# Performance work log

Hardware: AMD Instinct MI355X
Metric: run time of the kernel (lower is better)

The kernel has to match this reference:

```python
import jax, jax.numpy as jnp
import numpy as np

N = 50000          # nodes
E = 800000         # edges (before self-loops)
IN_CH = 128
HID = 64
HEADS = 4
NEG_SLOPE = 0.2    # PyG GATConv default negative_slope


def _gat_conv(x, W, a_src, a_dst, bias, src, dst, heads, out_ch):
    """PyG-style GATConv (concat=True). src/dst already include self-loops."""
    n = x.shape[0]
    h = (x @ W).reshape(n, heads, out_ch)                 # [N,H,C]
    # per-node attention halves: a_src . h_i  and  a_dst . h_i
    es = (h * a_src[None]).sum(-1)                        # [N,H]
    ed = (h * a_dst[None]).sum(-1)                        # [N,H]
    logits = jax.nn.leaky_relu(es[src] + ed[dst], NEG_SLOPE)   # [Etot,H]
    # segment softmax over incoming edges of each dst node
    m = jax.ops.segment_max(logits, dst, num_segments=n)       # [N,H]
    m = jnp.where(jnp.isfinite(m), m, jnp.zeros_like(m))
    p = jnp.exp(logits - m[dst])                               # [Etot,H]
    s = jax.ops.segment_sum(p, dst, num_segments=n)            # [N,H]
    att = p / (s[dst] + 1e-16)                                 # [Etot,H]
    msg = h[src] * att[..., None]                              # [Etot,H,C]
    out = jax.ops.segment_sum(msg, dst, num_segments=n)        # [N,H,C]
    return out.reshape(n, heads * out_ch) + bias


def setup_inputs() -> dict:
    key = jax.random.key(0)
    ks = jax.random.split(key, 12)
    x = jax.random.normal(ks[0], (N, IN_CH), dtype=jnp.float32)
    edge_index = jax.random.randint(ks[1], (2, E), 0, N, dtype=jnp.int32)
    def glorot(k, shape, fan_in):
        return jax.random.normal(k, shape, dtype=jnp.float32) * (1.0 / np.sqrt(fan_in))
    return {
        "x": x,
        "W1": glorot(ks[2], (IN_CH, HEADS * HID), IN_CH),
        "a_src1": glorot(ks[3], (HEADS, HID), HID),
        "a_dst1": glorot(ks[4], (HEADS, HID), HID),
        "b1": jnp.zeros((HEADS * HID,), dtype=jnp.float32),
        "W2": glorot(ks[5], (HEADS * HID, HID), HEADS * HID),
        "a_src2": glorot(ks[6], (1, HID), HID),
        "a_dst2": glorot(ks[7], (1, HID), HID),
        "b2": jnp.zeros((HID,), dtype=jnp.float32),
        "Wo": glorot(ks[8], (HID, 1), HID),
        "bo": jnp.zeros((1,), dtype=jnp.float32),
        "edge_index": edge_index,
    }


def reference(x, W1, a_src1, a_dst1, b1, W2, a_src2, a_dst2, b2, Wo, bo, edge_index):
    n = x.shape[0]
    loops = jnp.arange(n, dtype=edge_index.dtype)          # add_self_loops=True (PyG default)
    src = jnp.concatenate([edge_index[0], loops])
    dst = jnp.concatenate([edge_index[1], loops])
    h = jax.nn.elu(_gat_conv(x, W1, a_src1, a_dst1, b1, src, dst, HEADS, HID))
    # dropout inactive in eval mode
    h = jax.nn.elu(_gat_conv(h, W2, a_src2, a_dst2, b2, src, dst, 1, HID))
    return (h @ Wo + bo).squeeze(-1)                       # [N]
```

## Files before the change

### kernel.cpp

```cpp
#include <hip/hip_runtime.h>
#include <cmath>

#define LRELU_SLOPE 0.2f

static inline int cdiv_h(int a, int b){ return (a + b - 1) / b; }

__device__ __forceinline__ float dev_lrelu(float x){ return x > 0.f ? x : LRELU_SLOPE * x; }
__device__ __forceinline__ float dev_elu(float x){ return x > 0.f ? x : expm1f(x); }

__device__ __forceinline__ unsigned short f2bf(float f){
  unsigned int u = __float_as_uint(f);
  u = (u + 0x7FFFu + ((u >> 16) & 1u)) >> 16;
  return (unsigned short)u;
}
__device__ __forceinline__ float bf2f_lo(unsigned int u){
  return __uint_as_float(u << 16);
}
__device__ __forceinline__ float bf2f_hi(unsigned int u){
  return __uint_as_float(u & 0xFFFF0000u);
}

__device__ __forceinline__ float edge_w(float logit){
  return __expf(fminf(logit, 80.f));
}

typedef __attribute__((ext_vector_type(8))) short bf16x8;
typedef __attribute__((ext_vector_type(4))) float f32x4;

#define CNT_STRIDE 16

__global__ void prep_kernel(const float* __restrict__ W1, unsigned short* __restrict__ W1T,
                            const float* __restrict__ W2, unsigned short* __restrict__ W2T,
                            int* __restrict__ cnt, int n)
{
  int b = blockIdx.x, t = threadIdx.x;
  if (b < 128){
    int i = b * 256 + t;
    int k = i >> 8, c = i & 255;
    W1T[(size_t)c * 128 + k] = f2bf(W1[i]);
  } else if (b < 192){
    int i = (b - 128) * 256 + t;
    int k = i >> 6, c = i & 63;
    W2T[(size_t)c * 256 + k] = f2bf(W2[i]);
  } else {
    int i = (b - 192) * 256 + t;
    if (i < n) cnt[(size_t)i * CNT_STRIDE] = 1;
  }
}


__global__ void scan_blocks_kernel(const int* __restrict__ cnt, int* __restrict__ rowptr,
                                   int n, int* __restrict__ bsum){
  __shared__ int sd[256];
  int idx = blockIdx.x * 256 + threadIdx.x;
  int v = (idx < n) ? cnt[(size_t)idx * CNT_STRIDE] : 0;
  sd[threadIdx.x] = v;
  __syncthreads();
  #pragma unroll
  for (int off = 1; off < 256; off <<= 1){
    int x = (threadIdx.x >= off) ? sd[threadIdx.x - off] : 0;
    __syncthreads();
    sd[threadIdx.x] += x;
    __syncthreads();
  }
  if (idx < n) rowptr[idx] = sd[threadIdx.x] - v;
  if (threadIdx.x == 255) bsum[blockIdx.x] = sd[255];
}

__global__ void scan_add_kernel(int* __restrict__ rowptr, int n, const int* __restrict__ bsum,
                                int total, unsigned short* __restrict__ col){
  __shared__ int red[256];
  int t = threadIdx.x;
  int p = 0;
  for (int k = t; k < (int)blockIdx.x; k += 256) p += bsum[k];
  red[t] = p;
  __syncthreads();
  #pragma unroll
  for (int off = 128; off > 0; off >>= 1){
    if (t < off) red[t] += red[t + off];
    __syncthreads();
  }
  int prefix = red[0];
  int idx = blockIdx.x * 256 + t;
  if (idx < n){
    int v = rowptr[idx] + prefix;
    rowptr[idx] = v;
    col[v] = (unsigned short)idx;
  }
  if (idx == 0) rowptr[n] = total;
}

__global__ void scatter_kernel(const int* __restrict__ ei, const int* __restrict__ rank,
                               const int* __restrict__ rowptr, int e, unsigned short* __restrict__ col){
  int i = blockIdx.x * blockDim.x + threadIdx.x;
  if (i >= e) return;
  int s = ei[i], d = ei[e + i];
  col[rowptr[d] + rank[i]] = (unsigned short)s;
}

__launch_bounds__(256)
__global__ void gemm1_mfma_kernel(const float* __restrict__ A, const unsigned short* __restrict__ BT,
                                  unsigned short* __restrict__ Cb,
                                  const float* __restrict__ a_src, const float* __restrict__ a_dst,
                                  float* __restrict__ es, float* __restrict__ ed,
                                  int M, int K, int GB,
                                  const int* __restrict__ hist_dst, int He,
                                  int* __restrict__ cnt, int* __restrict__ rank)
{
  constexpr int BN = 256, NSUB = 16, H = 4;
  constexpr int LDK = 40;
  __shared__ short As[64 * LDK];
  __shared__ short Bs[BN * LDK];
  const int tid = threadIdx.x;

  if (blockIdx.x >= GB){
    int i = (blockIdx.x - GB) * 256 + tid;
    if (i < He){
      int d = hist_dst[i];
      rank[i] = atomicAdd(&cnt[(size_t)d * CNT_STRIDE], 1);
    }
    return;
  }

  const int bm = blockIdx.x;
  const int wave = tid >> 6, lane = tid & 63;
  const int lm = lane & 15, quad = lane >> 4;
  const int arow = tid >> 2, kc8 = (tid & 3) * 8;
  const int gm_a = bm * 64 + arow;

  f32x4 acc[NSUB];
  #pragma unroll
  for (int i = 0; i < NSUB; i++) acc[i] = (f32x4){0.f, 0.f, 0.f, 0.f};

  for (int k0 = 0; k0 < K; k0 += 32){
    unsigned short a8[8];
    float4 t0 = {0,0,0,0}, t1 = {0,0,0,0};
    if (gm_a < M){
      t0 = *(const float4*)&A[(size_t)gm_a * K + k0 + kc8];
      t1 = *(const float4*)&A[(size_t)gm_a * K + k0 + kc8 + 4];
    }
    a8[0] = f2bf(t0.x); a8[1] = f2bf(t0.y); a8[2] = f2bf(t0.z); a8[3] = f2bf(t0.w);
    a8[4] = f2bf(t1.x); a8[5] = f2bf(t1.y); a8[6] = f2bf(t1.z); a8[7] = f2bf(t1.w);
    uint4 b8[4];
    #pragma unroll
    for (int rep = 0; rep < 4; rep++){
      int brow = rep * 64 + arow;
      b8[rep] = *(const uint4*)&BT[(size_t)brow * K + k0 + kc8];
    }
    __syncthreads();
    *(uint4*)&As[arow * LDK + kc8] = *(uint4*)a8;
    #pragma unroll
    for (int rep = 0; rep < 4; rep++)
      *(uint4*)&Bs[(rep * 64 + arow) * LDK + kc8] = b8[rep];
    __syncthreads();
    bf16x8 af = *(const bf16x8*)&As[(wave * 16 + lm) * LDK + quad * 8];
    #pragma unroll
    for (int nb = 0; nb < NSUB; nb++){
      bf16x8 bfr = *(const bf16x8*)&Bs[(nb * 16 + lm) * LDK + quad * 8];
      acc[nb] = __builtin_amdgcn_mfma_f32_16x16x32_bf16(af, bfr, acc[nb], 0, 0, 0);
    }
  }

  float asv[NSUB], adv[NSUB];
  #pragma unroll
  for (int nb = 0; nb < NSUB; nb++){
    asv[nb] = a_src[nb * 16 + lm];
    adv[nb] = a_dst[nb * 16 + lm];
  }
  #pragma unroll
  for (int r = 0; r < 4; r++){
    int gm = bm * 64 + wave * 16 + quad * 4 + r;
    if (gm < M){
      #pragma unroll
      for (int nb = 0; nb < NSUB; nb++)
        Cb[(size_t)gm * BN + nb * 16 + lm] = f2bf(acc[nb][r]);
    }
    #pragma unroll
    for (int h = 0; h < H; h++){
      float ps = 0.f, pd = 0.f;
      #pragma unroll
      for (int nbh = 0; nbh < 4; nbh++){
        int nb = h * 4 + nbh;
        float a = acc[nb][r];
        ps += a * asv[nb];
        pd += a * adv[nb];
      }
      #pragma unroll
      for (int off = 1; off < 16; off <<= 1){
        ps += __shfl_xor(ps, off, 64);
        pd += __shfl_xor(pd, off, 64);
      }
      if (lm == 0 && gm < M){
        es[(size_t)gm * H + h] = ps;
        ed[(size_t)gm * H + h] = pd;
      }
    }
  }
}

__launch_bounds__(256)
__global__ void gemm2_mfma_kernel(const unsigned short* __restrict__ A, const unsigned short* __restrict__ BT,
                                  unsigned short* __restrict__ Cb,
                                  const float* __restrict__ a_src, const float* __restrict__ a_dst,
                                  float* __restrict__ es, float* __restrict__ ed,
                                  int M, int K)
{
  constexpr int BN = 64, NSUB = 4;
  constexpr int LDK = 40;
  __shared__ short As[128 * LDK];
  __shared__ short Bs[64 * LDK];
  const int tid = threadIdx.x;
  const int bm = blockIdx.x;
  const int wave = tid >> 6, lane = tid & 63;
  const int lm = lane & 15, quad = lane >> 4;
  const int arow = tid >> 2, kc8 = (tid & 3) * 8;
  const int gm_a0 = bm * 128 + arow;
  const int gm_a1 = gm_a0 + 64;

  f32x4 acc0[NSUB], acc1[NSUB];
  #pragma unroll
  for (int i = 0; i < NSUB; i++){
    acc0[i] = (f32x4){0.f, 0.f, 0.f, 0.f};
    acc1[i] = (f32x4){0.f, 0.f, 0.f, 0.f};
  }

  for (int k0 = 0; k0 < K; k0 += 32){
    uint4 a0 = make_uint4(0,0,0,0), a1 = make_uint4(0,0,0,0);
    if (gm_a0 < M) a0 = *(const uint4*)&A[(size_t)gm_a0 * K + k0 + kc8];
    if (gm_a1 < M) a1 = *(const uint4*)&A[(size_t)gm_a1 * K + k0 + kc8];
    uint4 b = *(const uint4*)&BT[(size_t)arow * K + k0 + kc8];
    __syncthreads();
    *(uint4*)&As[arow * LDK + kc8] = a0;
    *(uint4*)&As[(64 + arow) * LDK + kc8] = a1;
    *(uint4*)&Bs[arow * LDK + kc8] = b;
    __syncthreads();
    bf16x8 af0 = *(const bf16x8*)&As[(wave * 16 + lm) * LDK + quad * 8];
    bf16x8 af1 = *(const bf16x8*)&As[(64 + wave * 16 + lm) * LDK + quad * 8];
    #pragma unroll
    for (int nb = 0; nb < NSUB; nb++){
      bf16x8 bfr = *(const bf16x8*)&Bs[(nb * 16 + lm) * LDK + quad * 8];
      acc0[nb] = __builtin_amdgcn_mfma_f32_16x16x32_bf16(af0, bfr, acc0[nb], 0, 0, 0);
      acc1[nb] = __builtin_amdgcn_mfma_f32_16x16x32_bf16(af1, bfr, acc1[nb], 0, 0, 0);
    }
  }

  float asv[NSUB], adv[NSUB];
  #pragma unroll
  for (int nb = 0; nb < NSUB; nb++){
    asv[nb] = a_src[nb * 16 + lm];
    adv[nb] = a_dst[nb * 16 + lm];
  }
  #pragma unroll
  for (int half = 0; half < 2; half++){
    #pragma unroll
    for (int r = 0; r < 4; r++){
      int gm = bm * 128 + half * 64 + wave * 16 + quad * 4 + r;
      float ps = 0.f, pd = 0.f;
      #pragma unroll
      for (int nb = 0; nb < NSUB; nb++){
        float a = half ? acc1[nb][r] : acc0[nb][r];
        if (gm < M) Cb[(size_t)gm * BN + nb * 16 + lm] = f2bf(a);
        ps += a * asv[nb];
        pd += a * adv[nb];
      }
      #pragma unroll
      for (int off = 1; off < 16; off <<= 1){
        ps += __shfl_xor(ps, off, 64);
        pd += __shfl_xor(pd, off, 64);
      }
      if (lm == 0 && gm < M){
        es[gm] = ps;
        ed[gm] = pd;
      }
    }
  }
}

__global__ void agg1_kernel(const unsigned short* __restrict__ h1b, const float* __restrict__ es,
                            const float* __restrict__ ed,
                            const int* __restrict__ rowptr, const unsigned short* __restrict__ col,
                            const float* __restrict__ b1, unsigned short* __restrict__ out1b, int n)
{
  int node = blockIdx.x * 8 + (threadIdx.x >> 5);
  if (node >= n) return;
  int r = threadIdx.x & 31;
  int h = r >> 3;
  float edh = ed[node * 4 + h];
  int start = rowptr[node], end = rowptr[node + 1];
  float l = 0.f;
  float a0=0.f,a1=0.f,a2=0.f,a3=0.f,a4=0.f,a5=0.f,a6=0.f,a7=0.f;
  int j = start;
  for (; j + 3 < end; j += 4){
    int s0 = col[j], s1 = col[j+1], s2 = col[j+2], s3 = col[j+3];
    float e0 = es[s0*4 + h], e1 = es[s1*4 + h], e2 = es[s2*4 + h], e3 = es[s3*4 + h];
    uint4 r0 = *(const uint4*)&h1b[(size_t)s0 * 256 + r * 8];
    uint4 r1 = *(const uint4*)&h1b[(size_t)s1 * 256 + r * 8];
    uint4 r2 = *(const uint4*)&h1b[(size_t)s2 * 256 + r * 8];
    uint4 r3 = *(const uint4*)&h1b[(size_t)s3 * 256 + r * 8];
    float w0 = edge_w(dev_lrelu(e0 + edh));
    float w1 = edge_w(dev_lrelu(e1 + edh));
    float w2 = edge_w(dev_lrelu(e2 + edh));
    float w3 = edge_w(dev_lrelu(e3 + edh));
    l += w0 + w1 + w2 + w3;
    a0 += bf2f_lo(r0.x)*w0 + bf2f_lo(r1.x)*w1 + bf2f_lo(r2.x)*w2 + bf2f_lo(r3.x)*w3;
    a1 += bf2f_hi(r0.x)*w0 + bf2f_hi(r1.x)*w1 + bf2f_hi(r2.x)*w2 + bf2f_hi(r3.x)*w3;
    a2 += bf2f_lo(r0.y)*w0 + bf2f_lo(r1.y)*w1 + bf2f_lo(r2.y)*w2 + bf2f_lo(r3.y)*w3;
    a3 += bf2f_hi(r0.y)*w0 + bf2f_hi(r1.y)*w1 + bf2f_hi(r2.y)*w2 + bf2f_hi(r3.y)*w3;
    a4 += bf2f_lo(r0.z)*w0 + bf2f_lo(r1.z)*w1 + bf2f_lo(r2.z)*w2 + bf2f_lo(r3.z)*w3;
    a5 += bf2f_hi(r0.z)*w0 + bf2f_hi(r1.z)*w1 + bf2f_hi(r2.z)*w2 + bf2f_hi(r3.z)*w3;
    a6 += bf2f_lo(r0.w)*w0 + bf2f_lo(r1.w)*w1 + bf2f_lo(r2.w)*w2 + bf2f_lo(r3.w)*w3;
    a7 += bf2f_hi(r0.w)*w0 + bf2f_hi(r1.w)*w1 + bf2f_hi(r2.w)*w2 + bf2f_hi(r3.w)*w3;
  }
  for (; j < end; j++){
    int s0 = col[j];
    float w0 = edge_w(dev_lrelu(es[s0*4 + h] + edh));
    uint4 r0 = *(const uint4*)&h1b[(size_t)s0 * 256 + r * 8];
    l += w0;
    a0 += bf2f_lo(r0.x)*w0; a1 += bf2f_hi(r0.x)*w0;
    a2 += bf2f_lo(r0.y)*w0; a3 += bf2f_hi(r0.y)*w0;
    a4 += bf2f_lo(r0.z)*w0; a5 += bf2f_hi(r0.z)*w0;
    a6 += bf2f_lo(r0.w)*w0; a7 += bf2f_hi(r0.w)*w0;
  }
  float inv = 1.f / l;
  float4 bA = *(const float4*)&b1[r * 8];
  float4 bB = *(const float4*)&b1[r * 8 + 4];
  uint4 o;
  o.x = (unsigned int)f2bf(dev_elu(a0*inv + bA.x)) | ((unsigned int)f2bf(dev_elu(a1*inv + bA.y)) << 16);
  o.y = (unsigned int)f2bf(dev_elu(a2*inv + bA.z)) | ((unsigned int)f2bf(dev_elu(a3*inv + bA.w)) << 16);
  o.z = (unsigned int)f2bf(dev_elu(a4*inv + bB.x)) | ((unsigned int)f2bf(dev_elu(a5*inv + bB.y)) << 16);
  o.w = (unsigned int)f2bf(dev_elu(a6*inv + bB.z)) | ((unsigned int)f2bf(dev_elu(a7*inv + bB.w)) << 16);
  *(uint4*)&out1b[(size_t)node * 256 + r * 8] = o;
}

__global__ void agg2_kernel(const unsigned short* __restrict__ h2b, const float* __restrict__ es,
                            const float* __restrict__ ed,
                            const int* __restrict__ rowptr, const unsigned short* __restrict__ col,
                            const float* __restrict__ b2, const float* __restrict__ Wo,
                            const float* __restrict__ bo, float* __restrict__ out, int n)
{
  int node = blockIdx.x * 16 + (threadIdx.x >> 4);
  if (node >= n) return;
  int r = threadIdx.x & 15;
  float edh = ed[node];
  int start = rowptr[node], end = rowptr[node + 1];
  float l = 0.f;
  float a0=0.f,a1=0.f,a2=0.f,a3=0.f;
  int j = start;
  for (; j + 3 < end; j += 4){
    int s0 = col[j], s1 = col[j+1], s2 = col[j+2], s3 = col[j+3];
    float e0 = es[s0], e1 = es[s1], e2 = es[s2], e3 = es[s3];
    uint2 r0 = *(const uint2*)&h2b[(size_t)s0 * 64 + r * 4];
    uint2 r1 = *(const uint2*)&h2b[(size_t)s1 * 64 + r * 4];
    uint2 r2 = *(const uint2*)&h2b[(size_t)s2 * 64 + r * 4];
    uint2 r3 = *(const uint2*)&h2b[(size_t)s3 * 64 + r * 4];
    float w0 = edge_w(dev_lrelu(e0 + edh));
    float w1 = edge_w(dev_lrelu(e1 + edh));
    float w2 = edge_w(dev_lrelu(e2 + edh));
    float w3 = edge_w(dev_lrelu(e3 + edh));
    l += w0 + w1 + w2 + w3;
    a0 += bf2f_lo(r0.x)*w0 + bf2f_lo(r1.x)*w1 + bf2f_lo(r2.x)*w2 + bf2f_lo(r3.x)*w3;
    a1 += bf2f_hi(r0.x)*w0 + bf2f_hi(r1.x)*w1 + bf2f_hi(r2.x)*w2 + bf2f_hi(r3.x)*w3;
    a2 += bf2f_lo(r0.y)*w0 + bf2f_lo(r1.y)*w1 + bf2f_lo(r2.y)*w2 + bf2f_lo(r3.y)*w3;
    a3 += bf2f_hi(r0.y)*w0 + bf2f_hi(r1.y)*w1 + bf2f_hi(r2.y)*w2 + bf2f_hi(r3.y)*w3;
  }
  for (; j < end; j++){
    int s0 = col[j];
    float w0 = edge_w(dev_lrelu(es[s0] + edh));
    uint2 r0 = *(const uint2*)&h2b[(size_t)s0 * 64 + r * 4];
    l += w0;
    a0 += bf2f_lo(r0.x)*w0; a1 += bf2f_hi(r0.x)*w0;
    a2 += bf2f_lo(r0.y)*w0; a3 += bf2f_hi(r0.y)*w0;
  }
  float inv = 1.f / l;
  float4 bb = *(const float4*)&b2[r * 4];
  float4 wo = *(const float4*)&Wo[r * 4];
  float t = dev_elu(a0*inv + bb.x) * wo.x
          + dev_elu(a1*inv + bb.y) * wo.y
          + dev_elu(a2*inv + bb.z) * wo.z
          + dev_elu(a3*inv + bb.w) * wo.w;
  #pragma unroll
  for (int off = 1; off < 16; off <<= 1) t += __shfl_xor(t, off, 64);
  if (r == 0) out[node] = t + bo[0];
}

extern "C" void kernel_launch(void* const* d_in, const int* in_sizes, int n_in,
                              void* d_out, int out_size, void* d_ws, size_t ws_size,
                              hipStream_t stream)
{
  const float* x    = (const float*)d_in[0];
  const float* W1   = (const float*)d_in[1];
  const float* a_s1 = (const float*)d_in[2];
  const float* a_d1 = (const float*)d_in[3];
  const float* b1   = (const float*)d_in[4];
  const float* W2   = (const float*)d_in[5];
  const float* a_s2 = (const float*)d_in[6];
  const float* a_d2 = (const float*)d_in[7];
  const float* b2   = (const float*)d_in[8];
  const float* Wo   = (const float*)d_in[9];
  const float* bo   = (const float*)d_in[10];
  const int*   ei   = (const int*)d_in[11];

  const int Nn = in_sizes[0] / 128;
  const int E  = in_sizes[11] / 2;
  const int ET = E + Nn;

  size_t off = 0;
  auto carve = [&](size_t bytes) -> void* {
    void* p = (char*)d_ws + off;
    off += (bytes + 255) & ~(size_t)255;
    return p;
  };
  unsigned short* h1b   = (unsigned short*)carve((size_t)Nn * 256 * sizeof(unsigned short));
  unsigned short* out1b = (unsigned short*)carve((size_t)Nn * 256 * sizeof(unsigned short));
  unsigned short* h2b   = (unsigned short*)carve((size_t)Nn * 64 * sizeof(unsigned short));
  unsigned short* W1T   = (unsigned short*)carve((size_t)128 * 256 * sizeof(unsigned short));
  unsigned short* W2T   = (unsigned short*)carve((size_t)256 * 64 * sizeof(unsigned short));
  float* es1    = (float*)carve((size_t)Nn * 4 * sizeof(float));
  float* ed1    = (float*)carve((size_t)Nn * 4 * sizeof(float));
  float* es2    = (float*)carve((size_t)Nn * sizeof(float));
  float* ed2    = (float*)carve((size_t)Nn * sizeof(float));
  int*   cnt    = (int*)carve((size_t)Nn * CNT_STRIDE * sizeof(int));
  int*   rowptr = (int*)carve((size_t)(Nn + 1) * sizeof(int));
  int*   rank   = (int*)carve((size_t)E * sizeof(int));
  int*   bsum   = (int*)carve(256 * sizeof(int));
  unsigned short* col = (unsigned short*)carve((size_t)ET * sizeof(unsigned short));
  float* out = (float*)d_out;

  int deg_blocks = cdiv_h(Nn, 256);
  prep_kernel<<<192 + deg_blocks, 256, 0, stream>>>(W1, W1T, W2, W2T, cnt, Nn);

  int GB1 = cdiv_h(Nn, 64);
  int HB  = cdiv_h(E, 256);
  gemm1_mfma_kernel<<<GB1 + HB, 256, 0, stream>>>(
      x, W1T, h1b, a_s1, a_d1, es1, ed1, Nn, 128, GB1, ei + E, E, cnt, rank);

  int nb = cdiv_h(Nn, 256);
  scan_blocks_kernel<<<nb, 256, 0, stream>>>(cnt, rowptr, Nn, bsum);
  scan_add_kernel<<<nb, 256, 0, stream>>>(rowptr, Nn, bsum, ET, col);
  scatter_kernel<<<cdiv_h(E, 256), 256, 0, stream>>>(ei, rank, rowptr, E, col);

  agg1_kernel<<<cdiv_h(Nn, 8), 256, 0, stream>>>(h1b, es1, ed1, rowptr, col, b1, out1b, Nn);

  gemm2_mfma_kernel<<<cdiv_h(Nn, 128), 256, 0, stream>>>(
      out1b, W2T, h2b, a_s2, a_d2, es2, ed2, Nn, 256);
  agg2_kernel<<<cdiv_h(Nn, 16), 256, 0, stream>>>(h2b, es2, ed2, rowptr, col, b2, Wo, bo, out, Nn);
}
```

Measured before the change: 255.8 us.

## Build CSR with chunked shared-memory histograms instead of global atomics

Replaces the global-atomic degree counting and per-edge rank with a chunked approach. Per-chunk shared-memory histograms over node quarters are written as 16-bit counts, then a per-node scan across chunks gives offsets, and a placement pass recomputes local ranks with shared atomics. The histogram no longer overlaps with gemm1 and needs two edge passes plus an NC×N count array. Both edge passes run a 4×NC grid, so every edge is read four times. Self-loop placement uses the +1 offset.

Result: slower. 280.8 us (+9.8%).

```diff
diff --git a/kernel.cpp b/kernel.cpp
--- a/kernel.cpp
+++ b/kernel.cpp
@@ -27,33 +27,102 @@
 typedef __attribute__((ext_vector_type(8))) short bf16x8;
 typedef __attribute__((ext_vector_type(4))) float f32x4;
 
-#define CNT_STRIDE 16
+#define CE 8192
+#define QS 12500
 
 __global__ void prep_kernel(const float* __restrict__ W1, unsigned short* __restrict__ W1T,
-                            const float* __restrict__ W2, unsigned short* __restrict__ W2T,
-                            int* __restrict__ cnt, int n)
+                            const float* __restrict__ W2, unsigned short* __restrict__ W2T)
 {
   int b = blockIdx.x, t = threadIdx.x;
   if (b < 128){
     int i = b * 256 + t;
     int k = i >> 8, c = i & 255;
     W1T[(size_t)c * 128 + k] = f2bf(W1[i]);
-  } else if (b < 192){
+  } else {
     int i = (b - 128) * 256 + t;
     int k = i >> 6, c = i & 63;
     W2T[(size_t)c * 256 + k] = f2bf(W2[i]);
-  } else {
-    int i = (b - 192) * 256 + t;
-    if (i < n) cnt[(size_t)i * CNT_STRIDE] = 1;
-  }
-}
-
-
-__global__ void scan_blocks_kernel(const int* __restrict__ cnt, int* __restrict__ rowptr,
+  }
+}
+
+
+__global__ void csr_count_kernel(const int* __restrict__ dst, int e, int n,
+                                 unsigned short* __restrict__ cnt)
+{
+  __shared__ unsigned int lc[QS];
+  int c = blockIdx.x, q = blockIdx.y;
+  int lo = q * QS;
+  int hi = min(lo + QS, n);
+  int width = hi - lo;
+  for (int k = threadIdx.x; k < width; k += 256) lc[k] = 0;
+  __syncthreads();
+  int i0 = c * CE, i1 = min(i0 + CE, e);
+  for (int i = i0 + threadIdx.x; i < i1; i += 256){
+    int d = dst[i];
+    if (d >= lo && d < hi) atomicAdd(&lc[d - lo], 1u);
+  }
+  __syncthreads();
+  size_t base = (size_t)c * n + lo;
+  for (int k = threadIdx.x; k < width; k += 256) cnt[base + k] = (unsigned short)lc[k];
+}
+
+__global__ void csr_chunkscan_kernel(unsigned short* __restrict__ cnt, int NC, int n,
+                                     int* __restrict__ deg_tot)
+{
+  int d = blockIdx.x * 256 + threadIdx.x;
+  if (d >= n) return;
+  unsigned int acc = 0;
+  int c = 0;
+  for (; c + 3 < NC; c += 4){
+    size_t i0 = (size_t)(c+0) * n + d;
+    size_t i1 = (size_t)(c+1) * n + d;
+    size_t i2 = (size_t)(c+2) * n + d;
+    size_t i3 = (size_t)(c+3) * n + d;
+    unsigned int t0 = cnt[i0], t1 = cnt[i1], t2 = cnt[i2], t3 = cnt[i3];
+    cnt[i0] = (unsigned short)acc;
+    cnt[i1] = (unsigned short)(acc + t0);
+    cnt[i2] = (unsigned short)(acc + t0 + t1);
+    cnt[i3] = (unsigned short)(acc + t0 + t1 + t2);
+    acc += t0 + t1 + t2 + t3;
+  }
+  for (; c < NC; c++){
+    size_t i = (size_t)c * n + d;
+    unsigned int t = cnt[i];
+    cnt[i] = (unsigned short)acc;
+    acc += t;
+  }
+  deg_tot[d] = (int)acc + 1;
+}
+
+__global__ void csr_place_kernel(const int* __restrict__ ei, int e, int n,
+                                 const unsigned short* __restrict__ rel,
+                                 const int* __restrict__ rowptr,
+                                 unsigned short* __restrict__ col)
+{
+  __shared__ unsigned int lc[QS];
+  int c = blockIdx.x, q = blockIdx.y;
+  int lo = q * QS;
+  int hi = min(lo + QS, n);
+  int width = hi - lo;
+  for (int k = threadIdx.x; k < width; k += 256) lc[k] = 0;
+  __syncthreads();
+  int i0 = c * CE, i1 = min(i0 + CE, e);
+  for (int i = i0 + threadIdx.x; i < i1; i += 256){
+    int s = ei[i], d = ei[e + i];
+    if (d >= lo && d < hi){
+      unsigned int lr = atomicAdd(&lc[d - lo], 1u);
+      int pos = rowptr[d] + 1 + (int)rel[(size_t)c * n + d] + (int)lr;
+      col[pos] = (unsigned short)s;
+    }
+  }
+}
+
+
+__global__ void scan_blocks_kernel(const int* __restrict__ deg, int* __restrict__ rowptr,
                                    int n, int* __restrict__ bsum){
   __shared__ int sd[256];
   int idx = blockIdx.x * 256 + threadIdx.x;
-  int v = (idx < n) ? cnt[(size_t)idx * CNT_STRIDE] : 0;
+  int v = (idx < n) ? deg[idx] : 0;
   sd[threadIdx.x] = v;
   __syncthreads();
   #pragma unroll
@@ -90,38 +159,18 @@
   if (idx == 0) rowptr[n] = total;
 }
 
-__global__ void scatter_kernel(const int* __restrict__ ei, const int* __restrict__ rank,
-                               const int* __restrict__ rowptr, int e, unsigned short* __restrict__ col){
-  int i = blockIdx.x * blockDim.x + threadIdx.x;
-  if (i >= e) return;
-  int s = ei[i], d = ei[e + i];
-  col[rowptr[d] + rank[i]] = (unsigned short)s;
-}
-
 __launch_bounds__(256)
 __global__ void gemm1_mfma_kernel(const float* __restrict__ A, const unsigned short* __restrict__ BT,
                                   unsigned short* __restrict__ Cb,
                                   const float* __restrict__ a_src, const float* __restrict__ a_dst,
                                   float* __restrict__ es, float* __restrict__ ed,
-                                  int M, int K, int GB,
-                                  const int* __restrict__ hist_dst, int He,
-                                  int* __restrict__ cnt, int* __restrict__ rank)
+                                  int M, int K)
 {
   constexpr int BN = 256, NSUB = 16, H = 4;
   constexpr int LDK = 40;
   __shared__ short As[64 * LDK];
   __shared__ short Bs[BN * LDK];
   const int tid = threadIdx.x;
-
-  if (blockIdx.x >= GB){
-    int i = (blockIdx.x - GB) * 256 + tid;
-    if (i < He){
-      int d = hist_dst[i];
-      rank[i] = atomicAdd(&cnt[(size_t)d * CNT_STRIDE], 1);
-    }
-    return;
-  }
-
   const int bm = blockIdx.x;
   const int wave = tid >> 6, lane = tid & 63;
   const int lm = lane & 15, quad = lane >> 4;
@@ -403,6 +452,7 @@
   const int Nn = in_sizes[0] / 128;
   const int E  = in_sizes[11] / 2;
   const int ET = E + Nn;
+  const int NC = cdiv_h(E, CE);
 
   size_t off = 0;
   auto carve = [&](size_t bytes) -> void* {
@@ -419,25 +469,24 @@
   float* ed1    = (float*)carve((size_t)Nn * 4 * sizeof(float));
   float* es2    = (float*)carve((size_t)Nn * sizeof(float));
   float* ed2    = (float*)carve((size_t)Nn * sizeof(float));
-  int*   cnt    = (int*)carve((size_t)Nn * CNT_STRIDE * sizeof(int));
+  unsigned short* cnt = (unsigned short*)carve((size_t)NC * Nn * sizeof(unsigned short));
+  int*   deg    = (int*)carve((size_t)Nn * sizeof(int));
   int*   rowptr = (int*)carve((size_t)(Nn + 1) * sizeof(int));
-  int*   rank   = (int*)carve((size_t)E * sizeof(int));
   int*   bsum   = (int*)carve(256 * sizeof(int));
   unsigned short* col = (unsigned short*)carve((size_t)ET * sizeof(unsigned short));
   float* out = (float*)d_out;
 
-  int deg_blocks = cdiv_h(Nn, 256);
-  prep_kernel<<<192 + deg_blocks, 256, 0, stream>>>(W1, W1T, W2, W2T, cnt, Nn);
-
-  int GB1 = cdiv_h(Nn, 64);
-  int HB  = cdiv_h(E, 256);
-  gemm1_mfma_kernel<<<GB1 + HB, 256, 0, stream>>>(
-      x, W1T, h1b, a_s1, a_d1, es1, ed1, Nn, 128, GB1, ei + E, E, cnt, rank);
-
+  prep_kernel<<<192, 256, 0, stream>>>(W1, W1T, W2, W2T);
+
+  gemm1_mfma_kernel<<<cdiv_h(Nn, 64), 256, 0, stream>>>(
+      x, W1T, h1b, a_s1, a_d1, es1, ed1, Nn, 128);
+
+  csr_count_kernel<<<dim3(NC, 4), 256, 0, stream>>>(ei + E, E, Nn, cnt);
+  csr_chunkscan_kernel<<<cdiv_h(Nn, 256), 256, 0, stream>>>(cnt, NC, Nn, deg);
   int nb = cdiv_h(Nn, 256);
-  scan_blocks_kernel<<<nb, 256, 0, stream>>>(cnt, rowptr, Nn, bsum);
+  scan_blocks_kernel<<<nb, 256, 0, stream>>>(deg, rowptr, Nn, bsum);
   scan_add_kernel<<<nb, 256, 0, stream>>>(rowptr, Nn, bsum, ET, col);
-  scatter_kernel<<<cdiv_h(E, 256), 256, 0, stream>>>(ei, rank, rowptr, E, col);
+  csr_place_kernel<<<dim3(NC, 4), 256, 0, stream>>>(ei, E, Nn, cnt, rowptr, col);
 
   agg1_kernel<<<cdiv_h(Nn, 8), 256, 0, stream>>>(h1b, es1, ed1, rowptr, col, b1, out1b, Nn);
 
```
